# Kernel tuning notes

Measured on AMD Instinct MI355X. Metric: run time of the kernel, lower is better.

## Reference

```python
import jax, jax.numpy as jnp
import numpy as np

B, S, D_IN, D_OUT, H = 2, 2048, 1024, 1024, 16
HD = D_OUT // H

def setup_inputs() -> dict:
    key = jax.random.key(0)
    ks = jax.random.split(key, 6)
    sc_in = 1.0 / np.sqrt(D_IN)
    sc_out = 1.0 / np.sqrt(D_OUT)
    return {
        "x": jax.random.normal(ks[0], (B, S, D_IN), dtype=jnp.float32),
        "Wq": jax.random.uniform(ks[1], (D_IN, D_OUT), jnp.float32, -sc_in, sc_in),
        "Wk": jax.random.uniform(ks[2], (D_IN, D_OUT), jnp.float32, -sc_in, sc_in),
        "Wv": jax.random.uniform(ks[3], (D_IN, D_OUT), jnp.float32, -sc_in, sc_in),
        "Wo": jax.random.uniform(ks[4], (D_OUT, D_OUT), jnp.float32, -sc_out, sc_out),
        "bo": jax.random.uniform(ks[5], (D_OUT,), jnp.float32, -sc_out, sc_out),
    }

def reference(x, Wq, Wk, Wv, Wo, bo):
    b, s, _ = x.shape
    # QKV projections (no bias), split heads -> [b, h, s, hd]
    q = (x @ Wq).reshape(b, s, H, HD).transpose(0, 2, 1, 3)
    k = (x @ Wk).reshape(b, s, H, HD).transpose(0, 2, 1, 3)
    v = (x @ Wv).reshape(b, s, H, HD).transpose(0, 2, 1, 3)
    scores = jnp.einsum('bhqd,bhkd->bhqk', q, k)
    causal = jnp.triu(jnp.ones((s, s), dtype=bool), k=1)
    scores = jnp.where(causal, -jnp.inf, scores)
    w = jax.nn.softmax(scores / np.sqrt(HD), axis=-1)  # dropout p=0.0 -> identity
    ctx = jnp.einsum('bhqk,bhkd->bhqd', w, v)
    ctx = ctx.transpose(0, 2, 1, 3).reshape(b, s, D_OUT)
    return ctx @ Wo + bo
```

## Files before the change

### kernel.cpp

```cpp
#include <hip/hip_runtime.h>
#include <stdint.h>

typedef unsigned short u16;
typedef __attribute__((ext_vector_type(8))) short short8;
typedef __attribute__((ext_vector_type(4))) float floatx4;
typedef __attribute__((ext_vector_type(4))) u16 ushort4v;

typedef __attribute__((address_space(1))) const uint32_t gu32;
typedef __attribute__((address_space(3))) uint32_t lu32;

#define MFMA(a, b, c) __builtin_amdgcn_mfma_f32_16x16x32_bf16((a), (b), (c), 0, 0, 0)

__device__ __forceinline__ u16 f2bf(float f) {
    union { float f; uint32_t u; } x; x.f = f;
    uint32_t u = x.u;
    u += 0x7fffu + ((u >> 16) & 1u);
    return (u16)(u >> 16);
}

__device__ __forceinline__ void async16(u16* lds, const u16* g) {
    __builtin_amdgcn_global_load_lds((gu32*)g, (lu32*)lds, 16, 0, 0);
}

__global__ __launch_bounds__(256) void prep_kernel(
    const float* __restrict__ x,
    const float* __restrict__ W0, const float* __restrict__ W1,
    const float* __restrict__ W2, const float* __restrict__ W3,
    u16* __restrict__ WT, u16* __restrict__ Xbf)
{
    const int z = blockIdx.z;
    const int tx = threadIdx.x, ty = threadIdx.y;
    if (z == 4) {
        const int bid = blockIdx.y * 32 + blockIdx.x;
        const int t = ty * 32 + tx;
        const size_t base = ((size_t)bid * 256 + t) * 16;
        const float* xf = x + base;
        short8 v0, v1;
#pragma unroll
        for (int j = 0; j < 8; j++) v0[j] = (short)f2bf(xf[j]);
#pragma unroll
        for (int j = 0; j < 8; j++) v1[j] = (short)f2bf(xf[8 + j]);
        *(short8*)&Xbf[base] = v0;
        *(short8*)&Xbf[base + 8] = v1;
        return;
    }
    __shared__ u16 tile[32][33];
    const float* W = (z == 0) ? W0 : (z == 1) ? W1 : (z == 2) ? W2 : W3;
    u16* dst = WT + (size_t)z * 1024 * 1024;
    const int n0 = blockIdx.x * 32, k0 = blockIdx.y * 32;
#pragma unroll
    for (int i = 0; i < 4; i++)
        tile[ty + i * 8][tx] = f2bf(W[(size_t)(k0 + ty + i * 8) * 1024 + n0 + tx]);
    __syncthreads();
#pragma unroll
    for (int i = 0; i < 4; i++)
        dst[(size_t)(n0 + ty + i * 8) * 1024 + k0 + tx] = tile[tx][ty + i * 8];
}

__global__ __launch_bounds__(256) void gemm_qkv_kernel(
    const u16* __restrict__ X, const u16* __restrict__ WT,
    u16* __restrict__ Q, u16* __restrict__ Kout, u16* __restrict__ VT)
{
    __shared__ __align__(16) u16 As[128 * 32];
    __shared__ __align__(16) u16 Bs[128 * 32];
    const int bid = blockIdx.x;
    const int xcd = bid & 7;
    const int idx = bid >> 3;
    const int mat = idx >> 5;
    const int rr  = (idx >> 3) & 3;
    const int nn  = idx & 7;
    const int m0 = (xcd * 4 + rr) * 128;
    const int n0 = nn * 128;
    const u16* BW = WT + (size_t)mat * 1024 * 1024;
    const int tid = threadIdx.x;
    const int wave = tid >> 6, lane = tid & 63;
    const int lrow = lane & 15, lquad = lane >> 4;
    const int wr = (wave >> 1) * 64, wc = (wave & 1) * 64;

    const int ci0 = wave * 128 + lane;
    const int ci1 = ci0 + 64;
    const int ar0 = ci0 >> 2, ac0 = (ci0 & 3) * 8;
    const int ar1 = ci1 >> 2, ac1 = (ci1 & 3) * 8;
    u16* ldsA0 = As + (size_t)(wave * 128) * 8;
    u16* ldsA1 = As + (size_t)(wave * 128 + 64) * 8;
    u16* ldsB0 = Bs + (size_t)(wave * 128) * 8;
    u16* ldsB1 = Bs + (size_t)(wave * 128 + 64) * 8;
    const u16* gA0 = &X[(size_t)(m0 + ar0) * 1024 + ac0];
    const u16* gA1 = &X[(size_t)(m0 + ar1) * 1024 + ac1];
    const u16* gB0 = &BW[(size_t)(n0 + ar0) * 1024 + ac0];
    const u16* gB1 = &BW[(size_t)(n0 + ar1) * 1024 + ac1];

    floatx4 acc[4][4];
#pragma unroll
    for (int mt = 0; mt < 4; mt++)
#pragma unroll
        for (int nt = 0; nt < 4; nt++) acc[mt][nt] = (floatx4){0.f, 0.f, 0.f, 0.f};

    for (int k0 = 0; k0 < 1024; k0 += 32) {
        __syncthreads();
        async16(ldsA0, gA0 + k0);
        async16(ldsA1, gA1 + k0);
        async16(ldsB0, gB0 + k0);
        async16(ldsB1, gB1 + k0);
        __syncthreads();
        short8 af[4], bf[4];
#pragma unroll
        for (int mt = 0; mt < 4; mt++)
            af[mt] = *(const short8*)&As[(wr + mt * 16 + lrow) * 32 + lquad * 8];
#pragma unroll
        for (int nt = 0; nt < 4; nt++)
            bf[nt] = *(const short8*)&Bs[(wc + nt * 16 + lrow) * 32 + lquad * 8];
#pragma unroll
        for (int mt = 0; mt < 4; mt++)
#pragma unroll
            for (int nt = 0; nt < 4; nt++)
                acc[mt][nt] = MFMA(af[mt], bf[nt], acc[mt][nt]);
    }

#pragma unroll
    for (int mt = 0; mt < 4; mt++) {
        const int gm = m0 + wr + mt * 16 + lquad * 4;
        const int b_ = gm >> 11;
        const int s  = gm & 2047;
#pragma unroll
        for (int nt = 0; nt < 4; nt++) {
            const int gn = n0 + wc + nt * 16 + lrow;
            const int h = gn >> 6, hd = gn & 63;
            const int bh = b_ * 16 + h;
            if (mat == 2) {
                ushort4v v;
#pragma unroll
                for (int i = 0; i < 4; i++) v[i] = f2bf(acc[mt][nt][i]);
                *(ushort4v*)&VT[((size_t)bh * 64 + hd) * 2048 + s] = v;
            } else {
                u16* dst = (mat == 0) ? Q : Kout;
#pragma unroll
                for (int i = 0; i < 4; i++)
                    dst[((size_t)bh * 2048 + s + i) * 64 + hd] = f2bf(acc[mt][nt][i]);
            }
        }
    }
}

__global__ __launch_bounds__(256, 4) void attn_kernel(
    const u16* __restrict__ Q, const u16* __restrict__ Kk,
    const u16* __restrict__ VT, u16* __restrict__ ctx)
{
    __shared__ __align__(16) u16 Ks[64][72];
    __shared__ __align__(16) u16 Vs[64][72];
    __shared__ __align__(16) u16 P[4][16][72];
    const int tid = threadIdx.x, wave = tid >> 6, lane = tid & 63;
    const int lrow = lane & 15, lquad = lane >> 4;
    const float scale = 0.125f;
    const float NEGINF = -__builtin_inff();

    const int bh = blockIdx.x & 31;
    const int g = blockIdx.x >> 5;
    const int qb = (g < 16) ? (31 - g) : (g - 16);
    const int ntiles = qb + 1;
    const int q0 = qb * 64 + wave * 16;

    const u16* Qb = Q  + (size_t)bh * 2048 * 64;
    const u16* Kb = Kk + (size_t)bh * 2048 * 64;
    const u16* Vb = VT + (size_t)bh * 64 * 2048;

    const short8 qf0 = *(const short8*)&Qb[(size_t)(q0 + lrow) * 64 + lquad * 8];
    const short8 qf1 = *(const short8*)&Qb[(size_t)(q0 + lrow) * 64 + 32 + lquad * 8];

    const int myq = q0 + lrow;
    float m_s = NEGINF, l_s = 0.f;
    floatx4 o[4];
#pragma unroll
    for (int i = 0; i < 4; i++) o[i] = (floatx4){0.f, 0.f, 0.f, 0.f};

    const int r0 = tid >> 3, c0 = (tid & 7) * 8;
    const int r1 = (tid + 256) >> 3, c1 = c0;

    short8 kreg0 = *(const short8*)&Kb[(size_t)r0 * 64 + c0];
    short8 kreg1 = *(const short8*)&Kb[(size_t)r1 * 64 + c1];
    short8 vreg0 = *(const short8*)&Vb[(size_t)r0 * 2048 + c0];
    short8 vreg1 = *(const short8*)&Vb[(size_t)r1 * 2048 + c1];

    for (int kt = 0; kt < ntiles; kt++) {
        __syncthreads();
        *(short8*)&Ks[r0][c0] = kreg0;
        *(short8*)&Ks[r1][c1] = kreg1;
        *(short8*)&Vs[r0][c0] = vreg0;
        *(short8*)&Vs[r1][c1] = vreg1;
        if (kt + 1 < ntiles) {
            kreg0 = *(const short8*)&Kb[(size_t)((kt + 1) * 64 + r0) * 64 + c0];
            kreg1 = *(const short8*)&Kb[(size_t)((kt + 1) * 64 + r1) * 64 + c1];
            vreg0 = *(const short8*)&Vb[(size_t)r0 * 2048 + (kt + 1) * 64 + c0];
            vreg1 = *(const short8*)&Vb[(size_t)r1 * 2048 + (kt + 1) * 64 + c1];
        }
        __syncthreads();

        floatx4 s[4];
#pragma unroll
        for (int nt = 0; nt < 4; nt++) {
            const short8 kf0 = *(const short8*)&Ks[nt * 16 + lrow][lquad * 8];
            const short8 kf1 = *(const short8*)&Ks[nt * 16 + lrow][32 + lquad * 8];
            floatx4 a = (floatx4){0.f, 0.f, 0.f, 0.f};
            a = MFMA(kf0, qf0, a);
            a = MFMA(kf1, qf1, a);
            s[nt] = a;
        }

        const bool diag = (kt == ntiles - 1);
        float mx = NEGINF;
#pragma unroll
        for (int nt = 0; nt < 4; nt++)
#pragma unroll
            for (int i = 0; i < 4; i++) {
                float v = s[nt][i] * scale;
                if (diag && (kt * 64 + nt * 16 + lquad * 4 + i > myq)) v = NEGINF;
                s[nt][i] = v;
                mx = fmaxf(mx, v);
            }
        mx = fmaxf(mx, __shfl_xor(mx, 16));
        mx = fmaxf(mx, __shfl_xor(mx, 32));
        const float mnew = fmaxf(m_s, mx);
        const float alpha = __expf(m_s - mnew);
        m_s = mnew;
        float sum = 0.f;
#pragma unroll
        for (int nt = 0; nt < 4; nt++)
#pragma unroll
            for (int i = 0; i < 4; i++) {
                const float pv = __expf(s[nt][i] - mnew);
                s[nt][i] = pv;
                sum += pv;
            }
        sum += __shfl_xor(sum, 16);
        sum += __shfl_xor(sum, 32);
        l_s = l_s * alpha + sum;
#pragma unroll
        for (int ht = 0; ht < 4; ht++)
#pragma unroll
            for (int i = 0; i < 4; i++) o[ht][i] *= alpha;

#pragma unroll
        for (int nt = 0; nt < 4; nt++) {
            uint32_t pk0 = (uint32_t)f2bf(s[nt][0]) | ((uint32_t)f2bf(s[nt][1]) << 16);
            uint32_t pk1 = (uint32_t)f2bf(s[nt][2]) | ((uint32_t)f2bf(s[nt][3]) << 16);
            uint2 pk = {pk0, pk1};
            *(uint2*)&P[wave][lrow][nt * 16 + lquad * 4] = pk;
        }
#pragma unroll
        for (int st = 0; st < 2; st++) {
            const short8 pf = *(const short8*)&P[wave][lrow][st * 32 + lquad * 8];
#pragma unroll
            for (int ht = 0; ht < 4; ht++) {
                const short8 vf = *(const short8*)&Vs[ht * 16 + lrow][st * 32 + lquad * 8];
                o[ht] = MFMA(vf, pf, o[ht]);
            }
        }
    }

    const int b_ = bh >> 4, h_ = bh & 15;
    const float inv_l = 1.0f / l_s;
#pragma unroll
    for (int ht = 0; ht < 4; ht++) {
        uint32_t pk0 = (uint32_t)f2bf(o[ht][0] * inv_l) | ((uint32_t)f2bf(o[ht][1] * inv_l) << 16);
        uint32_t pk1 = (uint32_t)f2bf(o[ht][2] * inv_l) | ((uint32_t)f2bf(o[ht][3] * inv_l) << 16);
        uint2 pk = {pk0, pk1};
        *(uint2*)&ctx[((size_t)(b_ * 2048 + q0 + lrow)) * 1024 + h_ * 64 + ht * 16 + lquad * 4] = pk;
    }
}

__global__ __launch_bounds__(256) void gemm_out_kernel(
    const u16* __restrict__ X, const u16* __restrict__ WT,
    const float* __restrict__ bias, float* __restrict__ out)
{
    __shared__ __align__(16) u16 As[128 * 32];
    __shared__ __align__(16) u16 Bs[128 * 32];
    const int bid = blockIdx.x;
    const int xcd = bid & 7;
    const int idx = bid >> 3;
    const int rr  = idx >> 3;
    const int nn  = idx & 7;
    const int m0 = (xcd * 4 + rr) * 128;
    const int n0 = nn * 128;
    const int tid = threadIdx.x;
    const int wave = tid >> 6, lane = tid & 63;
    const int lrow = lane & 15, lquad = lane >> 4;
    const int wr = (wave >> 1) * 64, wc = (wave & 1) * 64;

    const int ci0 = wave * 128 + lane;
    const int ci1 = ci0 + 64;
    const int ar0 = ci0 >> 2, ac0 = (ci0 & 3) * 8;
    const int ar1 = ci1 >> 2, ac1 = (ci1 & 3) * 8;
    u16* ldsA0 = As + (size_t)(wave * 128) * 8;
    u16* ldsA1 = As + (size_t)(wave * 128 + 64) * 8;
    u16* ldsB0 = Bs + (size_t)(wave * 128) * 8;
    u16* ldsB1 = Bs + (size_t)(wave * 128 + 64) * 8;
    const u16* gA0 = &X[(size_t)(m0 + ar0) * 1024 + ac0];
    const u16* gA1 = &X[(size_t)(m0 + ar1) * 1024 + ac1];
    const u16* gB0 = &WT[(size_t)(n0 + ar0) * 1024 + ac0];
    const u16* gB1 = &WT[(size_t)(n0 + ar1) * 1024 + ac1];

    floatx4 acc[4][4];
#pragma unroll
    for (int mt = 0; mt < 4; mt++)
#pragma unroll
        for (int nt = 0; nt < 4; nt++) acc[mt][nt] = (floatx4){0.f, 0.f, 0.f, 0.f};

    for (int k0 = 0; k0 < 1024; k0 += 32) {
        __syncthreads();
        async16(ldsA0, gA0 + k0);
        async16(ldsA1, gA1 + k0);
        async16(ldsB0, gB0 + k0);
        async16(ldsB1, gB1 + k0);
        __syncthreads();
        short8 af[4], bf[4];
#pragma unroll
        for (int mt = 0; mt < 4; mt++)
            af[mt] = *(const short8*)&As[(wr + mt * 16 + lrow) * 32 + lquad * 8];
#pragma unroll
        for (int nt = 0; nt < 4; nt++)
            bf[nt] = *(const short8*)&Bs[(wc + nt * 16 + lrow) * 32 + lquad * 8];
#pragma unroll
        for (int mt = 0; mt < 4; mt++)
#pragma unroll
            for (int nt = 0; nt < 4; nt++)
                acc[mt][nt] = MFMA(af[mt], bf[nt], acc[mt][nt]);
    }

#pragma unroll
    for (int mt = 0; mt < 4; mt++) {
        const int gm = m0 + wr + mt * 16 + lquad * 4;
#pragma unroll
        for (int nt = 0; nt < 4; nt++) {
            const int gn = n0 + wc + nt * 16 + lrow;
            const float bv = bias[gn];
#pragma unroll
            for (int i = 0; i < 4; i++)
                out[(size_t)(gm + i) * 1024 + gn] = acc[mt][nt][i] + bv;
        }
    }
}

extern "C" void kernel_launch(void* const* d_in, const int* in_sizes, int n_in,
                              void* d_out, int out_size, void* d_ws, size_t ws_size,
                              hipStream_t stream) {
    u16* ws = (u16*)d_ws + 64;

    const size_t MB1 = 1024 * 1024;
    u16* WT   = ws;
    u16* Qw   = ws + 4 * MB1;
    u16* Kw   = ws + 8 * MB1;
    u16* VTw  = ws + 12 * MB1;
    u16* ctxw = ws + 16 * MB1;
    u16* Xbf  = ws + 20 * MB1;

    prep_kernel<<<dim3(32, 32, 5), dim3(32, 8), 0, stream>>>(
        (const float*)d_in[0], (const float*)d_in[1], (const float*)d_in[2],
        (const float*)d_in[3], (const float*)d_in[4], WT, Xbf);
    gemm_qkv_kernel<<<768, 256, 0, stream>>>(Xbf, WT, Qw, Kw, VTw);
    attn_kernel<<<1024, 256, 0, stream>>>(Qw, Kw, VTw, ctxw);
    gemm_out_kernel<<<256, 256, 0, stream>>>(ctxw, WT + 3 * MB1, (const float*)d_in[5], (float*)d_out);
}
```

Baseline: 183.9 us.

## Fold softmax scale into Q, use exp2, lazy rescale, swizzled LDS, packed bf16 converts

The softmax scale and log2(e) are folded into Q in the projection epilogue, so the attention loop drops the per-element multiply and uses a native exp2. The running-max rescale of the output accumulator is skipped unless some lane's max grows by more than a threshold (a lazy rescale). K and V tiles in LDS move from padded rows to an XOR-swizzled 128-byte-row layout to avoid bank conflicts without padding. The bit-twiddling bf16 conversions are replaced with the hardware packed-convert instruction. The trade-offs are extra branch divergence checks, bounded but larger intermediate exponent ranges, and a dependence on the target supporting v_cvt_pk_bf16_f32.

```diff
diff --git a/kernel.cpp b/kernel.cpp
--- a/kernel.cpp
+++ b/kernel.cpp
@@ -18,9 +18,32 @@
     return (u16)(u >> 16);
 }
 
+__device__ __forceinline__ uint32_t cvtpk_bf16(float lo, float hi) {
+    uint32_t r;
+    asm("v_cvt_pk_bf16_f32 %0, %1, %2" : "=v"(r) : "v"(lo), "v"(hi));
+    return r;
+}
+
+__device__ __forceinline__ float fexp2(float x) {
+#if defined(__has_builtin)
+#if __has_builtin(__builtin_amdgcn_exp2f)
+    return __builtin_amdgcn_exp2f(x);
+#else
+    return exp2f(x);
+#endif
+#else
+    return exp2f(x);
+#endif
+}
+
 __device__ __forceinline__ void async16(u16* lds, const u16* g) {
     __builtin_amdgcn_global_load_lds((gu32*)g, (lu32*)lds, 16, 0, 0);
 }
+
+#define KV8(buf, row, byteInRow) \
+    (*(short8*)((char*)(buf) + (((row) << 7) + ((byteInRow) ^ (((row) & 7) << 4)))))
+
+#define Q_SCALE_LOG2E 0.18033688011112042f
 
 __global__ __launch_bounds__(256) void prep_kernel(
     const float* __restrict__ x,
@@ -117,6 +140,7 @@
                 acc[mt][nt] = MFMA(af[mt], bf[nt], acc[mt][nt]);
     }
 
+    const float qs = (mat == 0) ? Q_SCALE_LOG2E : 1.0f;
 #pragma unroll
     for (int mt = 0; mt < 4; mt++) {
         const int gm = m0 + wr + mt * 16 + lquad * 4;
@@ -136,7 +160,7 @@
                 u16* dst = (mat == 0) ? Q : Kout;
 #pragma unroll
                 for (int i = 0; i < 4; i++)
-                    dst[((size_t)bh * 2048 + s + i) * 64 + hd] = f2bf(acc[mt][nt][i]);
+                    dst[((size_t)bh * 2048 + s + i) * 64 + hd] = f2bf(acc[mt][nt][i] * qs);
             }
         }
     }
@@ -146,12 +170,11 @@
     const u16* __restrict__ Q, const u16* __restrict__ Kk,
     const u16* __restrict__ VT, u16* __restrict__ ctx)
 {
-    __shared__ __align__(16) u16 Ks[64][72];
-    __shared__ __align__(16) u16 Vs[64][72];
-    __shared__ __align__(16) u16 P[4][16][72];
+    __shared__ __align__(16) u16 Ks[64 * 64];
+    __shared__ __align__(16) u16 Vs[64 * 64];
+    __shared__ __align__(16) u16 P[4][16][80];
     const int tid = threadIdx.x, wave = tid >> 6, lane = tid & 63;
     const int lrow = lane & 15, lquad = lane >> 4;
-    const float scale = 0.125f;
     const float NEGINF = -__builtin_inff();
 
     const int bh = blockIdx.x & 31;
@@ -173,77 +196,85 @@
 #pragma unroll
     for (int i = 0; i < 4; i++) o[i] = (floatx4){0.f, 0.f, 0.f, 0.f};
 
-    const int r0 = tid >> 3, c0 = (tid & 7) * 8;
-    const int r1 = (tid + 256) >> 3, c1 = c0;
-
-    short8 kreg0 = *(const short8*)&Kb[(size_t)r0 * 64 + c0];
-    short8 kreg1 = *(const short8*)&Kb[(size_t)r1 * 64 + c1];
-    short8 vreg0 = *(const short8*)&Vb[(size_t)r0 * 2048 + c0];
-    short8 vreg1 = *(const short8*)&Vb[(size_t)r1 * 2048 + c1];
+    const int r0 = tid >> 3, r1 = r0 + 32;
+    const int ce = (tid & 7) * 8;
+    const int cb = (tid & 7) * 16;
+
+    short8 kreg0 = *(const short8*)&Kb[(size_t)r0 * 64 + ce];
+    short8 kreg1 = *(const short8*)&Kb[(size_t)r1 * 64 + ce];
+    short8 vreg0 = *(const short8*)&Vb[(size_t)r0 * 2048 + ce];
+    short8 vreg1 = *(const short8*)&Vb[(size_t)r1 * 2048 + ce];
 
     for (int kt = 0; kt < ntiles; kt++) {
         __syncthreads();
-        *(short8*)&Ks[r0][c0] = kreg0;
-        *(short8*)&Ks[r1][c1] = kreg1;
-        *(short8*)&Vs[r0][c0] = vreg0;
-        *(short8*)&Vs[r1][c1] = vreg1;
+        KV8(Ks, r0, cb) = kreg0;
+        KV8(Ks, r1, cb) = kreg1;
+        KV8(Vs, r0, cb) = vreg0;
+        KV8(Vs, r1, cb) = vreg1;
         if (kt + 1 < ntiles) {
-            kreg0 = *(const short8*)&Kb[(size_t)((kt + 1) * 64 + r0) * 64 + c0];
-            kreg1 = *(const short8*)&Kb[(size_t)((kt + 1) * 64 + r1) * 64 + c1];
-            vreg0 = *(const short8*)&Vb[(size_t)r0 * 2048 + (kt + 1) * 64 + c0];
-            vreg1 = *(const short8*)&Vb[(size_t)r1 * 2048 + (kt + 1) * 64 + c1];
+            kreg0 = *(const short8*)&Kb[(size_t)((kt + 1) * 64 + r0) * 64 + ce];
+            kreg1 = *(const short8*)&Kb[(size_t)((kt + 1) * 64 + r1) * 64 + ce];
+            vreg0 = *(const short8*)&Vb[(size_t)r0 * 2048 + (kt + 1) * 64 + ce];
+            vreg1 = *(const short8*)&Vb[(size_t)r1 * 2048 + (kt + 1) * 64 + ce];
         }
         __syncthreads();
 
         floatx4 s[4];
 #pragma unroll
         for (int nt = 0; nt < 4; nt++) {
-            const short8 kf0 = *(const short8*)&Ks[nt * 16 + lrow][lquad * 8];
-            const short8 kf1 = *(const short8*)&Ks[nt * 16 + lrow][32 + lquad * 8];
+            const short8 kf0 = KV8(Ks, nt * 16 + lrow, lquad * 16);
+            const short8 kf1 = KV8(Ks, nt * 16 + lrow, 64 + lquad * 16);
             floatx4 a = (floatx4){0.f, 0.f, 0.f, 0.f};
             a = MFMA(kf0, qf0, a);
             a = MFMA(kf1, qf1, a);
             s[nt] = a;
         }
 
-        const bool diag = (kt == ntiles - 1);
+        if (kt == ntiles - 1) {
+#pragma unroll
+            for (int nt = 0; nt < 4; nt++)
+#pragma unroll
+                for (int i = 0; i < 4; i++)
+                    if (kt * 64 + nt * 16 + lquad * 4 + i > myq) s[nt][i] = NEGINF;
+        }
+
         float mx = NEGINF;
 #pragma unroll
         for (int nt = 0; nt < 4; nt++)
-#pragma unroll
-            for (int i = 0; i < 4; i++) {
-                float v = s[nt][i] * scale;
-                if (diag && (kt * 64 + nt * 16 + lquad * 4 + i > myq)) v = NEGINF;
-                s[nt][i] = v;
-                mx = fmaxf(mx, v);
-            }
+            mx = fmaxf(mx, fmaxf(fmaxf(s[nt][0], s[nt][1]),
+                                 fmaxf(s[nt][2], s[nt][3])));
         mx = fmaxf(mx, __shfl_xor(mx, 16));
         mx = fmaxf(mx, __shfl_xor(mx, 32));
-        const float mnew = fmaxf(m_s, mx);
-        const float alpha = __expf(m_s - mnew);
-        m_s = mnew;
+
+        if (!__all(mx <= m_s + 8.0f)) {
+            const float mnew = fmaxf(m_s, mx);
+            const float alpha = fexp2(m_s - mnew);
+            m_s = mnew;
+            l_s *= alpha;
+#pragma unroll
+            for (int ht = 0; ht < 4; ht++)
+#pragma unroll
+                for (int i = 0; i < 4; i++) o[ht][i] *= alpha;
+        }
+
         float sum = 0.f;
 #pragma unroll
         for (int nt = 0; nt < 4; nt++)
 #pragma unroll
             for (int i = 0; i < 4; i++) {
-                const float pv = __expf(s[nt][i] - mnew);
+                const float pv = fexp2(s[nt][i] - m_s);
                 s[nt][i] = pv;
                 sum += pv;
             }
         sum += __shfl_xor(sum, 16);
         sum += __shfl_xor(sum, 32);
-        l_s = l_s * alpha + sum;
-#pragma unroll
-        for (int ht = 0; ht < 4; ht++)
-#pragma unroll
-            for (int i = 0; i < 4; i++) o[ht][i] *= alpha;
+        l_s += sum;
 
 #pragma unroll
         for (int nt = 0; nt < 4; nt++) {
-            uint32_t pk0 = (uint32_t)f2bf(s[nt][0]) | ((uint32_t)f2bf(s[nt][1]) << 16);
-            uint32_t pk1 = (uint32_t)f2bf(s[nt][2]) | ((uint32_t)f2bf(s[nt][3]) << 16);
-            uint2 pk = {pk0, pk1};
+            uint2 pk;
+            pk.x = cvtpk_bf16(s[nt][0], s[nt][1]);
+            pk.y = cvtpk_bf16(s[nt][2], s[nt][3]);
             *(uint2*)&P[wave][lrow][nt * 16 + lquad * 4] = pk;
         }
 #pragma unroll
@@ -251,7 +282,7 @@
             const short8 pf = *(const short8*)&P[wave][lrow][st * 32 + lquad * 8];
 #pragma unroll
             for (int ht = 0; ht < 4; ht++) {
-                const short8 vf = *(const short8*)&Vs[ht * 16 + lrow][st * 32 + lquad * 8];
+                const short8 vf = KV8(Vs, ht * 16 + lrow, st * 64 + lquad * 16);
                 o[ht] = MFMA(vf, pf, o[ht]);
             }
         }
@@ -261,9 +292,9 @@
     const float inv_l = 1.0f / l_s;
 #pragma unroll
     for (int ht = 0; ht < 4; ht++) {
-        uint32_t pk0 = (uint32_t)f2bf(o[ht][0] * inv_l) | ((uint32_t)f2bf(o[ht][1] * inv_l) << 16);
-        uint32_t pk1 = (uint32_t)f2bf(o[ht][2] * inv_l) | ((uint32_t)f2bf(o[ht][3] * inv_l) << 16);
-        uint2 pk = {pk0, pk1};
+        uint2 pk;
+        pk.x = cvtpk_bf16(o[ht][0] * inv_l, o[ht][1] * inv_l);
+        pk.y = cvtpk_bf16(o[ht][2] * inv_l, o[ht][3] * inv_l);
         *(uint2*)&ctx[((size_t)(b_ * 2048 + q0 + lrow)) * 1024 + h_ * 64 + ht * 16 + lquad * 4] = pk;
     }
 }
```

Result: slower. 191.7 us (+4.2%).
